# Kernel tuning notes

Measured on AMD Instinct MI355X. Metric: run time of the kernel, lower is better.

The kernel has to match this reference:

```python
import jax, jax.numpy as jnp
import numpy as np

THR = 0.2          # config['thr']
BORDER = 2         # config['border_rm']
H0C, W0C = 60, 80  # coarse grid of image0 (L = 4800)
H1C, W1C = 60, 80  # coarse grid of image1 (S = 4800)
TEMP_INIT = 10.0


def _border_mask():
    # valid (non-border) positions of the [h0,w0,h1,w1] grid, flattened to [L,S]
    def ok(n):
        a = jnp.arange(n)
        return (a >= BORDER) & (a < n - BORDER)
    m = (ok(H0C)[:, None, None, None] & ok(W0C)[None, :, None, None]
         & ok(H1C)[None, None, :, None] & ok(W1C)[None, None, None, :])
    return m.reshape(H0C * W0C, H1C * W1C)


def setup_inputs() -> dict:
    key = jax.random.key(0)
    k0, k1 = jax.random.split(key)
    feat_c0 = jax.random.normal(k0, (2, 4800, 256), dtype=jnp.float32)
    feat_c1 = jax.random.normal(k1, (2, 4800, 256), dtype=jnp.float32)
    temperature = jnp.asarray(TEMP_INIT, dtype=jnp.float32)
    return {"feat_c0": feat_c0, "feat_c1": feat_c1, "temperature": temperature}


def reference(feat_c0, feat_c1, temperature):
    C = feat_c0.shape[-1]
    inv_sqrt_c = 1.0 / float(C) ** 0.5
    f0 = feat_c0 * inv_sqrt_c
    f1 = feat_c1 * inv_sqrt_c
    # dense similarity GEMM: [N,L,S]
    sim = jnp.einsum('nlc,nsc->nls', f0, f1) * temperature
    # dual softmax -> confidence matrix
    conf = jax.nn.softmax(sim, axis=1) * jax.nn.softmax(sim, axis=2)
    # threshold + border removal (mask_border with b=BORDER)
    mask = (conf > THR) & _border_mask()[None]
    # mutual nearest neighbor
    mutual = (mask
              & (conf == conf.max(axis=2, keepdims=True))
              & (conf == conf.max(axis=1, keepdims=True)))
    # dense mconf map: conf at selected matches, 0 elsewhere (fixed-shape
    # equivalent of the b_ids/i_ids/j_ids nonzero extraction)
    mconf = jnp.where(mutual, conf, jnp.zeros((), conf.dtype))
    return conf, mconf
```

## Files before the change

### kernel.cpp

```cpp
#include <hip/hip_runtime.h>

#define L 4800
#define CH 256
#define NB 2
#define TT 38
#define NBL (NB * L)
#define THRF 0.2f

typedef float f32x4 __attribute__((ext_vector_type(4)));
typedef _Float16 h16;
typedef _Float16 h16x4 __attribute__((ext_vector_type(4)));
typedef _Float16 h16x8 __attribute__((ext_vector_type(8)));

__global__ __launch_bounds__(256) void convert_kernel(
    const float* __restrict__ f0, const float* __restrict__ f1,
    h16* __restrict__ A, h16* __restrict__ B)
{
    int idx = blockIdx.x * 256 + threadIdx.x;
    if (idx >= NB * L * CH / 4) return;
    f32x4 a = ((const f32x4*)f0)[idx];
    f32x4 b = ((const f32x4*)f1)[idx];
    h16x4 ah, bh;
#pragma unroll
    for (int k = 0; k < 4; ++k) { ah[k] = (h16)a[k]; bh[k] = (h16)b[k]; }
    ((h16x4*)A)[idx] = ah;
    ((h16x4*)B)[idx] = bh;
}

__global__ __launch_bounds__(256) void gemm_pass1(
    const h16* __restrict__ A, const h16* __restrict__ B,
    const float* __restrict__ temp,
    float* __restrict__ rs_part, float* __restrict__ cs_part)
{
    __shared__ __align__(16) h16 As[128 * 32];
    __shared__ __align__(16) h16 Bs[128 * 32];
    __shared__ float rp_lds[128][2];
    __shared__ float cp_lds[128][2];
    int bid = blockIdx.x;
    int n = bid / (TT * TT);
    int t = bid % (TT * TT);
    int tm = (t / TT) * 128;
    int tn = (t % TT) * 128;
    const h16* Ab = A + (long)n * L * CH;
    const h16* Bb = B + (long)n * L * CH;
    int tid = threadIdx.x;
    int lane = tid & 63;
    int w = tid >> 6;
    int wr = (w >> 1) * 64;
    int wc = (w & 1) * 64;

    f32x4 acc[4][4] = {};
    int lrow = lane >> 2;
    int kc8 = (lane & 3) * 8;

    for (int k0 = 0; k0 < CH; k0 += 32) {
        __syncthreads();
#pragma unroll
        for (int j = 0; j < 2; ++j) {
            int c = w * 2 + j;
            int row = c * 16 + lrow;
            int ga = tm + row; ga = ga > L - 1 ? L - 1 : ga;
            int gb = tn + row; gb = gb > L - 1 ? L - 1 : gb;
            __builtin_amdgcn_global_load_lds(
                (const __attribute__((address_space(1))) void*)(Ab + (long)ga * CH + k0 + kc8),
                (__attribute__((address_space(3))) void*)(As + c * 512), 16, 0, 0);
            __builtin_amdgcn_global_load_lds(
                (const __attribute__((address_space(1))) void*)(Bb + (long)gb * CH + k0 + kc8),
                (__attribute__((address_space(3))) void*)(Bs + c * 512), 16, 0, 0);
        }
        __syncthreads();

        h16x8 af[4], bf[4];
        int klo = (lane >> 4) * 8;
        int ra = wr + (lane & 15);
        int rb = wc + (lane & 15);
#pragma unroll
        for (int m = 0; m < 4; ++m) af[m] = *(const h16x8*)&As[(ra + m * 16) * 32 + klo];
#pragma unroll
        for (int nf = 0; nf < 4; ++nf) bf[nf] = *(const h16x8*)&Bs[(rb + nf * 16) * 32 + klo];
#pragma unroll
        for (int m = 0; m < 4; ++m)
#pragma unroll
            for (int nf = 0; nf < 4; ++nf)
                acc[m][nf] = __builtin_amdgcn_mfma_f32_16x16x32_f16(af[m], bf[nf], acc[m][nf], 0, 0, 0);
    }

    float scale = temp[0] * (1.0f / 256.0f);
    float rpart[4][4];
#pragma unroll
    for (int m = 0; m < 4; ++m)
#pragma unroll
        for (int j = 0; j < 4; ++j) rpart[m][j] = 0.f;
    float cpart[4] = {0.f, 0.f, 0.f, 0.f};
    int row0 = tm + wr + ((lane >> 4) * 4);
    int col0 = tn + wc + (lane & 15);
#pragma unroll
    for (int m = 0; m < 4; ++m)
#pragma unroll
        for (int nf = 0; nf < 4; ++nf)
#pragma unroll
            for (int j = 0; j < 4; ++j) {
                int rr = row0 + m * 16 + j;
                int cc = col0 + nf * 16;
                float e = 0.f;
                if (rr < L && cc < L) e = __expf(acc[m][nf][j] * scale);
                rpart[m][j] += e;
                cpart[nf] += e;
            }
#pragma unroll
    for (int m = 0; m < 4; ++m)
#pragma unroll
        for (int j = 0; j < 4; ++j) {
            float v = rpart[m][j];
            v += __shfl_xor(v, 1); v += __shfl_xor(v, 2);
            v += __shfl_xor(v, 4); v += __shfl_xor(v, 8);
            if ((lane & 15) == 0)
                rp_lds[wr + (lane >> 4) * 4 + m * 16 + j][w & 1] = v;
        }
#pragma unroll
    for (int nf = 0; nf < 4; ++nf) {
        float v = cpart[nf];
        v += __shfl_xor(v, 16); v += __shfl_xor(v, 32);
        if (lane < 16)
            cp_lds[wc + lane + nf * 16][w >> 1] = v;
    }
    __syncthreads();
    if (tid < 128) {
        int rr = tm + tid;
        if (rr < L)
            rs_part[(long)(t % TT) * NBL + n * L + rr] = rp_lds[tid][0] + rp_lds[tid][1];
    } else {
        int c2 = tid - 128;
        int cc = tn + c2;
        if (cc < L)
            cs_part[(long)(t / TT) * NBL + n * L + cc] = cp_lds[c2][0] + cp_lds[c2][1];
    }
}

__global__ __launch_bounds__(256) void reduce_inv(
    const float* __restrict__ rs_part, const float* __restrict__ cs_part,
    float* __restrict__ inv_rs, float* __restrict__ inv_cs)
{
    int i = blockIdx.x * 256 + threadIdx.x;
    if (i < NBL) {
        float s = 0.f;
        for (int t = 0; t < TT; ++t) s += rs_part[(long)t * NBL + i];
        inv_rs[i] = 1.0f / s;
    } else if (i < 2 * NBL) {
        int b = i - NBL;
        float s = 0.f;
        for (int t = 0; t < TT; ++t) s += cs_part[(long)t * NBL + b];
        inv_cs[b] = 1.0f / s;
    }
}

__global__ __launch_bounds__(256) void gemm_pass2(
    const h16* __restrict__ A, const h16* __restrict__ B,
    const float* __restrict__ temp,
    const float* __restrict__ inv_rs, const float* __restrict__ inv_cs,
    float* __restrict__ conf, float* __restrict__ mconf,
    float* __restrict__ rm_part, float* __restrict__ cm_part)
{
    __shared__ __align__(16) h16 As[128 * 32];
    __shared__ __align__(16) h16 Bs[128 * 32];
    __shared__ float rp_lds[128][2];
    __shared__ float cp_lds[128][2];
    int bid = blockIdx.x;
    int n = bid / (TT * TT);
    int t = bid % (TT * TT);
    int tm = (t / TT) * 128;
    int tn = (t % TT) * 128;
    const h16* Ab = A + (long)n * L * CH;
    const h16* Bb = B + (long)n * L * CH;
    int tid = threadIdx.x;
    int lane = tid & 63;
    int w = tid >> 6;
    int wr = (w >> 1) * 64;
    int wc = (w & 1) * 64;

    f32x4 acc[4][4] = {};
    int lrow = lane >> 2;
    int kc8 = (lane & 3) * 8;

    for (int k0 = 0; k0 < CH; k0 += 32) {
        __syncthreads();
#pragma unroll
        for (int j = 0; j < 2; ++j) {
            int c = w * 2 + j;
            int row = c * 16 + lrow;
            int ga = tm + row; ga = ga > L - 1 ? L - 1 : ga;
            int gb = tn + row; gb = gb > L - 1 ? L - 1 : gb;
            __builtin_amdgcn_global_load_lds(
                (const __attribute__((address_space(1))) void*)(Ab + (long)ga * CH + k0 + kc8),
                (__attribute__((address_space(3))) void*)(As + c * 512), 16, 0, 0);
            __builtin_amdgcn_global_load_lds(
                (const __attribute__((address_space(1))) void*)(Bb + (long)gb * CH + k0 + kc8),
                (__attribute__((address_space(3))) void*)(Bs + c * 512), 16, 0, 0);
        }
        __syncthreads();

        h16x8 af[4], bf[4];
        int klo = (lane >> 4) * 8;
        int ra = wr + (lane & 15);
        int rb = wc + (lane & 15);
#pragma unroll
        for (int m = 0; m < 4; ++m) af[m] = *(const h16x8*)&As[(ra + m * 16) * 32 + klo];
#pragma unroll
        for (int nf = 0; nf < 4; ++nf) bf[nf] = *(const h16x8*)&Bs[(rb + nf * 16) * 32 + klo];
#pragma unroll
        for (int m = 0; m < 4; ++m)
#pragma unroll
            for (int nf = 0; nf < 4; ++nf)
                acc[m][nf] = __builtin_amdgcn_mfma_f32_16x16x32_f16(af[m], bf[nf], acc[m][nf], 0, 0, 0);
    }

    float scale = temp[0] * (1.0f / 256.0f);
    int row0 = tm + wr + ((lane >> 4) * 4);
    int col0 = tn + wc + (lane & 15);
    float ics[4];
#pragma unroll
    for (int nf = 0; nf < 4; ++nf) {
        int cc = col0 + nf * 16;
        ics[nf] = (cc < L) ? inv_cs[n * L + cc] : 0.f;
    }
    float cmax[4] = {0.f, 0.f, 0.f, 0.f};
#pragma unroll
    for (int m = 0; m < 4; ++m)
#pragma unroll
        for (int j = 0; j < 4; ++j) {
            int rr = row0 + m * 16 + j;
            float irs_v = (rr < L) ? inv_rs[n * L + rr] : 0.f;
            float rm = 0.f;
#pragma unroll
            for (int nf = 0; nf < 4; ++nf) {
                int cc = col0 + nf * 16;
                if (rr < L && cc < L) {
                    float e = __expf(acc[m][nf][j] * scale);
                    float c = (e * e) * irs_v * ics[nf];
                    conf[((long)n * L + rr) * L + cc] = c;
                    rm = fmaxf(rm, c);
                    cmax[nf] = fmaxf(cmax[nf], c);
                }
            }
            rm = fmaxf(rm, __shfl_xor(rm, 1)); rm = fmaxf(rm, __shfl_xor(rm, 2));
            rm = fmaxf(rm, __shfl_xor(rm, 4)); rm = fmaxf(rm, __shfl_xor(rm, 8));
            if ((lane & 15) == 0)
                rp_lds[wr + (lane >> 4) * 4 + m * 16 + j][w & 1] = rm;
        }
#pragma unroll
    for (int nf = 0; nf < 4; ++nf) {
        float v = cmax[nf];
        v = fmaxf(v, __shfl_xor(v, 16)); v = fmaxf(v, __shfl_xor(v, 32));
        if (lane < 16)
            cp_lds[wc + lane + nf * 16][w >> 1] = v;
    }
    __syncthreads();
    if (tid < 128) {
        int rr = tm + tid;
        if (rr < L)
            rm_part[(long)(t % TT) * NBL + n * L + rr] = fmaxf(rp_lds[tid][0], rp_lds[tid][1]);
    } else {
        int c2 = tid - 128;
        int cc = tn + c2;
        if (cc < L)
            cm_part[(long)(t / TT) * NBL + n * L + cc] = fmaxf(cp_lds[c2][0], cp_lds[c2][1]);
    }

    f32x4 z = {0.f, 0.f, 0.f, 0.f};
    for (int i = tid; i < 128 * 32; i += 256) {
        int r = i >> 5;
        int cv = (i & 31) * 4;
        int rr = tm + r, cc = tn + cv;
        if (rr < L && cc + 3 < L)
            *(f32x4*)&mconf[((long)n * L + rr) * L + cc] = z;
    }
}

__global__ __launch_bounds__(256) void reduce_max(
    const float* __restrict__ rm_part, const float* __restrict__ cm_part,
    float* __restrict__ rowmaxf, float* __restrict__ colmaxf)
{
    int i = blockIdx.x * 256 + threadIdx.x;
    if (i < NBL) {
        float m = 0.f;
        for (int t = 0; t < TT; ++t) m = fmaxf(m, rm_part[(long)t * NBL + i]);
        rowmaxf[i] = m;
    } else if (i < 2 * NBL) {
        int b = i - NBL;
        float m = 0.f;
        for (int t = 0; t < TT; ++t) m = fmaxf(m, cm_part[(long)t * NBL + b]);
        colmaxf[b] = m;
    }
}

__global__ __launch_bounds__(256) void mconf_rows(
    const float* __restrict__ conf, const float* __restrict__ rowmaxf,
    const float* __restrict__ colmaxf, float* __restrict__ mconf)
{
    int b = blockIdx.x;
    float rmax = rowmaxf[b];
    if (!(rmax > THRF)) return;
    int l = b % L;
    int h0 = l / 80, w0 = l % 80;
    if (!((h0 >= 2) && (h0 < 58) && (w0 >= 2) && (w0 < 78))) return;
    int n = b / L;
    const float* Crow = conf + (long)b * L;
    for (int s = threadIdx.x; s < L; s += 256) {
        float c = Crow[s];
        if (c > THRF && c == rmax && c == colmaxf[n * L + s]) {
            int h1 = s / 80, w1 = s % 80;
            if ((h1 >= 2) && (h1 < 58) && (w1 >= 2) && (w1 < 78))
                mconf[(long)b * L + s] = c;
        }
    }
}

extern "C" void kernel_launch(void* const* d_in, const int* in_sizes, int n_in,
                              void* d_out, int out_size, void* d_ws, size_t ws_size,
                              hipStream_t stream)
{
    const float* f0 = (const float*)d_in[0];
    const float* f1 = (const float*)d_in[1];
    const float* temp = (const float*)d_in[2];

    float* conf  = (float*)d_out;
    float* mconf = conf + (long)NB * L * L;

    float* inv_rs  = (float*)d_ws;
    float* inv_cs  = inv_rs + NBL;
    float* rowmaxf = inv_cs + NBL;
    float* colmaxf = rowmaxf + NBL;
    float* rs_part = colmaxf + NBL;
    float* cs_part = rs_part + (long)TT * NBL;
    float* rm_part = cs_part + (long)TT * NBL;
    float* cm_part = rm_part + (long)TT * NBL;
    h16*   Abf     = (h16*)(cm_part + (long)TT * NBL);
    h16*   Bbf     = Abf + (long)NB * L * CH;

    convert_kernel<<<(NB * L * CH / 4 + 255) / 256, 256, 0, stream>>>(f0, f1, Abf, Bbf);
    gemm_pass1<<<NB * TT * TT, 256, 0, stream>>>(Abf, Bbf, temp, rs_part, cs_part);
    reduce_inv<<<(2 * NBL + 255) / 256, 256, 0, stream>>>(rs_part, cs_part, inv_rs, inv_cs);
    gemm_pass2<<<NB * TT * TT, 256, 0, stream>>>(Abf, Bbf, temp, inv_rs, inv_cs,
                                                 conf, mconf, rm_part, cm_part);
    reduce_max<<<(2 * NBL + 255) / 256, 256, 0, stream>>>(rm_part, cm_part, rowmaxf, colmaxf);
    mconf_rows<<<NBL, 256, 0, stream>>>(conf, rowmaxf, colmaxf, mconf);
}
```

Baseline: 475.2 us.

## Transpose MFMA operands for vectorized conf stores and move mconf zeroing to pass1

Swaps the MFMA A/B operands so each lane holds four consecutive columns of one row, letting pass2 write conf with 16-byte vector stores and load inv_cs as float4. The row and column reduction shuffles are remapped to the new fragment layout. Zero-filling mconf moves from pass2 into pass1, which only reads, to spread write traffic across both passes. The risk is that the vector store guard only checks ccb < L, which relies on L being a multiple of 4.

```diff
diff --git a/kernel.cpp b/kernel.cpp
--- a/kernel.cpp
+++ b/kernel.cpp
@@ -30,7 +30,8 @@
 __global__ __launch_bounds__(256) void gemm_pass1(
     const h16* __restrict__ A, const h16* __restrict__ B,
     const float* __restrict__ temp,
-    float* __restrict__ rs_part, float* __restrict__ cs_part)
+    float* __restrict__ rs_part, float* __restrict__ cs_part,
+    float* __restrict__ mconf)
 {
     __shared__ __align__(16) h16 As[128 * 32];
     __shared__ __align__(16) h16 Bs[128 * 32];
@@ -82,48 +83,44 @@
         for (int m = 0; m < 4; ++m)
 #pragma unroll
             for (int nf = 0; nf < 4; ++nf)
-                acc[m][nf] = __builtin_amdgcn_mfma_f32_16x16x32_f16(af[m], bf[nf], acc[m][nf], 0, 0, 0);
+                acc[m][nf] = __builtin_amdgcn_mfma_f32_16x16x32_f16(bf[nf], af[m], acc[m][nf], 0, 0, 0);
     }
 
     float scale = temp[0] * (1.0f / 256.0f);
-    float rpart[4][4];
-#pragma unroll
-    for (int m = 0; m < 4; ++m)
-#pragma unroll
-        for (int j = 0; j < 4; ++j) rpart[m][j] = 0.f;
-    float cpart[4] = {0.f, 0.f, 0.f, 0.f};
-    int row0 = tm + wr + ((lane >> 4) * 4);
-    int col0 = tn + wc + (lane & 15);
-#pragma unroll
-    for (int m = 0; m < 4; ++m)
-#pragma unroll
-        for (int nf = 0; nf < 4; ++nf)
+    int lr = lane & 15;
+    int lc4 = (lane >> 4) * 4;
+    float rowp[4] = {0.f, 0.f, 0.f, 0.f};
+    f32x4 colp[4] = {};
+#pragma unroll
+    for (int m = 0; m < 4; ++m) {
+        int rr = tm + wr + m * 16 + lr;
+#pragma unroll
+        for (int nf = 0; nf < 4; ++nf) {
+            int ccb = tn + wc + nf * 16 + lc4;
 #pragma unroll
             for (int j = 0; j < 4; ++j) {
-                int rr = row0 + m * 16 + j;
-                int cc = col0 + nf * 16;
                 float e = 0.f;
-                if (rr < L && cc < L) e = __expf(acc[m][nf][j] * scale);
-                rpart[m][j] += e;
-                cpart[nf] += e;
+                if (rr < L && (ccb + j) < L) e = __expf(acc[m][nf][j] * scale);
+                rowp[m] += e;
+                colp[nf][j] += e;
             }
-#pragma unroll
-    for (int m = 0; m < 4; ++m)
+        }
+    }
+#pragma unroll
+    for (int m = 0; m < 4; ++m) {
+        float v = rowp[m];
+        v += __shfl_xor(v, 16); v += __shfl_xor(v, 32);
+        if (lane < 16) rp_lds[wr + m * 16 + lr][w & 1] = v;
+    }
+#pragma unroll
+    for (int nf = 0; nf < 4; ++nf)
 #pragma unroll
         for (int j = 0; j < 4; ++j) {
-            float v = rpart[m][j];
+            float v = colp[nf][j];
             v += __shfl_xor(v, 1); v += __shfl_xor(v, 2);
             v += __shfl_xor(v, 4); v += __shfl_xor(v, 8);
-            if ((lane & 15) == 0)
-                rp_lds[wr + (lane >> 4) * 4 + m * 16 + j][w & 1] = v;
-        }
-#pragma unroll
-    for (int nf = 0; nf < 4; ++nf) {
-        float v = cpart[nf];
-        v += __shfl_xor(v, 16); v += __shfl_xor(v, 32);
-        if (lane < 16)
-            cp_lds[wc + lane + nf * 16][w >> 1] = v;
-    }
+            if ((lane & 15) == 0) cp_lds[wc + nf * 16 + lc4 + j][w >> 1] = v;
+        }
     __syncthreads();
     if (tid < 128) {
         int rr = tm + tid;
@@ -135,6 +132,15 @@
         if (cc < L)
             cs_part[(long)(t / TT) * NBL + n * L + cc] = cp_lds[c2][0] + cp_lds[c2][1];
     }
+
+    f32x4 z = {0.f, 0.f, 0.f, 0.f};
+    for (int i = tid; i < 128 * 32; i += 256) {
+        int r = i >> 5;
+        int cv = (i & 31) * 4;
+        int rr = tm + r, cc = tn + cv;
+        if (rr < L && cc < L)
+            *(f32x4*)&mconf[((long)n * L + rr) * L + cc] = z;
+    }
 }
 
 __global__ __launch_bounds__(256) void reduce_inv(
@@ -158,7 +164,7 @@
     const h16* __restrict__ A, const h16* __restrict__ B,
     const float* __restrict__ temp,
     const float* __restrict__ inv_rs, const float* __restrict__ inv_cs,
-    float* __restrict__ conf, float* __restrict__ mconf,
+    float* __restrict__ conf,
     float* __restrict__ rm_part, float* __restrict__ cm_part)
 {
     __shared__ __align__(16) h16 As[128 * 32];
@@ -211,49 +217,56 @@
         for (int m = 0; m < 4; ++m)
 #pragma unroll
             for (int nf = 0; nf < 4; ++nf)
-                acc[m][nf] = __builtin_amdgcn_mfma_f32_16x16x32_f16(af[m], bf[nf], acc[m][nf], 0, 0, 0);
+                acc[m][nf] = __builtin_amdgcn_mfma_f32_16x16x32_f16(bf[nf], af[m], acc[m][nf], 0, 0, 0);
     }
 
     float scale = temp[0] * (1.0f / 256.0f);
-    int row0 = tm + wr + ((lane >> 4) * 4);
-    int col0 = tn + wc + (lane & 15);
-    float ics[4];
+    int lr = lane & 15;
+    int lc4 = (lane >> 4) * 4;
+    f32x4 ics4[4];
 #pragma unroll
     for (int nf = 0; nf < 4; ++nf) {
-        int cc = col0 + nf * 16;
-        ics[nf] = (cc < L) ? inv_cs[n * L + cc] : 0.f;
-    }
-    float cmax[4] = {0.f, 0.f, 0.f, 0.f};
-#pragma unroll
-    for (int m = 0; m < 4; ++m)
+        int ccb = tn + wc + nf * 16 + lc4;
+        if (ccb < L) ics4[nf] = *(const f32x4*)&inv_cs[n * L + ccb];
+        else { ics4[nf][0] = 0.f; ics4[nf][1] = 0.f; ics4[nf][2] = 0.f; ics4[nf][3] = 0.f; }
+    }
+    float rowm[4] = {0.f, 0.f, 0.f, 0.f};
+    f32x4 colm[4] = {};
+#pragma unroll
+    for (int m = 0; m < 4; ++m) {
+        int rr = tm + wr + m * 16 + lr;
+        float irs_v = (rr < L) ? inv_rs[n * L + rr] : 0.f;
+#pragma unroll
+        for (int nf = 0; nf < 4; ++nf) {
+            int ccb = tn + wc + nf * 16 + lc4;
+            f32x4 cv;
+#pragma unroll
+            for (int j = 0; j < 4; ++j) {
+                float e = __expf(acc[m][nf][j] * scale);
+                float c = (e * e) * irs_v * ics4[nf][j];
+                cv[j] = c;
+                rowm[m] = fmaxf(rowm[m], c);
+                colm[nf][j] = fmaxf(colm[nf][j], c);
+            }
+            if (rr < L && ccb < L)
+                *(f32x4*)&conf[((long)n * L + rr) * L + ccb] = cv;
+        }
+    }
+#pragma unroll
+    for (int m = 0; m < 4; ++m) {
+        float v = rowm[m];
+        v = fmaxf(v, __shfl_xor(v, 16)); v = fmaxf(v, __shfl_xor(v, 32));
+        if (lane < 16) rp_lds[wr + m * 16 + lr][w & 1] = v;
+    }
+#pragma unroll
+    for (int nf = 0; nf < 4; ++nf)
 #pragma unroll
         for (int j = 0; j < 4; ++j) {
-            int rr = row0 + m * 16 + j;
-            float irs_v = (rr < L) ? inv_rs[n * L + rr] : 0.f;
-            float rm = 0.f;
-#pragma unroll
-            for (int nf = 0; nf < 4; ++nf) {
-                int cc = col0 + nf * 16;
-                if (rr < L && cc < L) {
-                    float e = __expf(acc[m][nf][j] * scale);
-                    float c = (e * e) * irs_v * ics[nf];
-                    conf[((long)n * L + rr) * L + cc] = c;
-                    rm = fmaxf(rm, c);
-                    cmax[nf] = fmaxf(cmax[nf], c);
-                }
-            }
-            rm = fmaxf(rm, __shfl_xor(rm, 1)); rm = fmaxf(rm, __shfl_xor(rm, 2));
-            rm = fmaxf(rm, __shfl_xor(rm, 4)); rm = fmaxf(rm, __shfl_xor(rm, 8));
-            if ((lane & 15) == 0)
-                rp_lds[wr + (lane >> 4) * 4 + m * 16 + j][w & 1] = rm;
-        }
-#pragma unroll
-    for (int nf = 0; nf < 4; ++nf) {
-        float v = cmax[nf];
-        v = fmaxf(v, __shfl_xor(v, 16)); v = fmaxf(v, __shfl_xor(v, 32));
-        if (lane < 16)
-            cp_lds[wc + lane + nf * 16][w >> 1] = v;
-    }
+            float v = colm[nf][j];
+            v = fmaxf(v, __shfl_xor(v, 1)); v = fmaxf(v, __shfl_xor(v, 2));
+            v = fmaxf(v, __shfl_xor(v, 4)); v = fmaxf(v, __shfl_xor(v, 8));
+            if ((lane & 15) == 0) cp_lds[wc + nf * 16 + lc4 + j][w >> 1] = v;
+        }
     __syncthreads();
     if (tid < 128) {
         int rr = tm + tid;
@@ -264,15 +277,6 @@
         int cc = tn + c2;
         if (cc < L)
             cm_part[(long)(t / TT) * NBL + n * L + cc] = fmaxf(cp_lds[c2][0], cp_lds[c2][1]);
-    }
-
-    f32x4 z = {0.f, 0.f, 0.f, 0.f};
-    for (int i = tid; i < 128 * 32; i += 256) {
-        int r = i >> 5;
-        int cv = (i & 31) * 4;
-        int rr = tm + r, cc = tn + cv;
-        if (rr < L && cc + 3 < L)
-            *(f32x4*)&mconf[((long)n * L + rr) * L + cc] = z;
     }
 }
 
@@ -338,10 +342,10 @@
     h16*   Bbf     = Abf + (long)NB * L * CH;
 
     convert_kernel<<<(NB * L * CH / 4 + 255) / 256, 256, 0, stream>>>(f0, f1, Abf, Bbf);
-    gemm_pass1<<<NB * TT * TT, 256, 0, stream>>>(Abf, Bbf, temp, rs_part, cs_part);
+    gemm_pass1<<<NB * TT * TT, 256, 0, stream>>>(Abf, Bbf, temp, rs_part, cs_part, mconf);
     reduce_inv<<<(2 * NBL + 255) / 256, 256, 0, stream>>>(rs_part, cs_part, inv_rs, inv_cs);
     gemm_pass2<<<NB * TT * TT, 256, 0, stream>>>(Abf, Bbf, temp, inv_rs, inv_cs,
-                                                 conf, mconf, rm_part, cm_part);
+                                                 conf, rm_part, cm_part);
     reduce_max<<<(2 * NBL + 255) / 256, 256, 0, stream>>>(rm_part, cm_part, rowmaxf, colmaxf);
     mconf_rows<<<NBL, 256, 0, stream>>>(conf, rowmaxf, colmaxf, mconf);
 }
```

Result: no change. 469.8 us (-1.1%).
